# Performance work log

Hardware: AMD Instinct MI355X
Metric: run time of the kernel (lower is better)

Reference implementation:

```python
import jax, jax.numpy as jnp
import numpy as np

B, T, D, E, K, OUT = 512, 2048, 32, 64, 8, 1024  # batch, tokens, feat(=32 hardcoded), experts, top-k, expert out dim


def setup_inputs() -> dict:
    key = jax.random.key(0)
    k0, k1, k2, k3 = jax.random.split(key, 4)
    x = jax.random.normal(k0, (B, T, D), jnp.float32)
    gate_w = jax.random.normal(k1, (E, D), jnp.float32) / np.sqrt(D)
    gate_b = jnp.zeros((E,), jnp.float32)
    # stacked expert Linear(32*k -> OUT): weight [E, OUT, D*K], bias [E, OUT]
    expert_w = jax.random.normal(k2, (E, OUT, D * K), jnp.float32) / np.sqrt(D * K)
    expert_b = jnp.zeros((E, OUT), jnp.float32)
    # gumbel noise for multinomial-without-replacement sampling (Gumbel top-k trick)
    gumbel = jax.random.gumbel(k3, (B, E, T), jnp.float32)
    return {"x": x, "gate_w": gate_w, "gate_b": gate_b,
            "expert_w": expert_w, "expert_b": expert_b, "gumbel": gumbel}


def reference(x, gate_w, gate_b, expert_w, expert_b, gumbel):
    # gate logits [B,T,E]; softmax over TOKEN axis (dim=-2 in torch)
    logits = jnp.einsum('btd,ed->bte', x, gate_w) + gate_b
    logp = jax.nn.log_softmax(logits, axis=-2)          # [B,T,E]
    # g = probs transposed to [B,E,T]; multinomial(k, no replacement) == top-k of log p + Gumbel
    scores = jnp.transpose(logp, (0, 2, 1)) + gumbel    # [B,E,T]
    _, idx = jax.lax.top_k(scores, K)                   # [B,E,K] sampled token indices
    # gather k tokens per (batch, expert): [B,E,K,D]
    gathered = jnp.take_along_axis(x[:, None, :, :], idx[..., None], axis=2)
    inp = gathered.reshape(B, E, K * D)                 # token-major concat, matches torch reshape
    # grouped per-expert GEMM + bias -> [B,E,OUT]
    out = jnp.einsum('bef,eof->beo', inp, expert_w) + expert_b[None]
    return out
```

## Files before the change

### kernel.cpp

```cpp
#include <hip/hip_runtime.h>
#include <hip/hip_bf16.h>
#include <stdint.h>

#define Bb   512
#define Tt   2048
#define Dd   32
#define Ee   64
#define Kk   8
#define OUTn 1024

typedef __attribute__((ext_vector_type(4))) float f32x4;
typedef __attribute__((ext_vector_type(8))) short short8;
typedef __attribute__((ext_vector_type(4))) unsigned int uint4v;

static __device__ __forceinline__ uint32_t f2bf(float f) {
  uint32_t u = __float_as_uint(f);
  return (u + 0x7FFFu + ((u >> 16) & 1u)) >> 16;
}
static __device__ __forceinline__ uint32_t umax32(uint32_t a, uint32_t b){ return a > b ? a : b; }
static __device__ __forceinline__ uint32_t umin32(uint32_t a, uint32_t b){ return a < b ? a : b; }

__global__ __launch_bounds__(1024) void kA_select(
    const float* __restrict__ x,
    const float* __restrict__ gate_w,
    const float* __restrict__ gumbel,
    uint16_t* __restrict__ inp)
{
  const int b    = blockIdx.x;
  const int tid  = threadIdx.x;
  const int wave = tid >> 6;
  const int lane = tid & 63;
  const int l15  = lane & 15;
  const int l4   = lane >> 4;
  const int c    = wave & 3;
  const int q    = wave >> 2;

  __shared__ __attribute__((aligned(16))) float gbuf[16 * 1024];
  __shared__ uint32_t cand[Ee][32];

  short8 gfrag;
  {
    const float* gp = gate_w + (size_t)(c * 16 + l15) * Dd + l4 * 8;
    f32x4 g0 = *(const f32x4*)(gp);
    f32x4 g1 = *(const f32x4*)(gp + 4);
    gfrag[0] = (short)f2bf(g0[0]); gfrag[1] = (short)f2bf(g0[1]);
    gfrag[2] = (short)f2bf(g0[2]); gfrag[3] = (short)f2bf(g0[3]);
    gfrag[4] = (short)f2bf(g1[0]); gfrag[5] = (short)f2bf(g1[1]);
    gfrag[6] = (short)f2bf(g1[2]); gfrag[7] = (short)f2bf(g1[3]);
  }

  uint32_t s[4][8];
  #pragma unroll
  for (int r = 0; r < 4; ++r)
    #pragma unroll
    for (int j = 0; j < 8; ++j) s[r][j] = 0u;

  const float* gchunk = gumbel + ((size_t)b * Ee + c * 16) * Tt + q * 512;
  const int v0 = (lane >> 5) * Tt + (lane & 31);
  const int v1 = (lane >> 5) * Tt + ((lane & 31) ^ 16);
  const float* xq = x + ((size_t)b * Tt + q * 512 + l15) * Dd + l4 * 8;

  auto stage = [&](int st, int bf) {
    #pragma unroll
    for (int j = 0; j < 8; ++j) {
      const float* src = gchunk + j * 2 * Tt + st * 32 + (((j >> 1) & 1) ? v1 : v0);
      float* dst = &gbuf[wave * 1024 + bf * 512 + j * 64];
      __builtin_amdgcn_global_load_lds(
          (const __attribute__((address_space(1))) void*)src,
          (__attribute__((address_space(3))) void*)dst, 4, 0, 0);
    }
  };

  auto compute = [&](int st, int bf, f32x4 (&xv)[4]) {
    const int sbase = wave * 1024 + bf * 512;
    #pragma unroll
    for (int g = 0; g < 2; ++g) {
      f32x4 lo = xv[g * 2], hi = xv[g * 2 + 1];
      short8 bfr;
      bfr[0] = (short)f2bf(lo[0]); bfr[1] = (short)f2bf(lo[1]);
      bfr[2] = (short)f2bf(lo[2]); bfr[3] = (short)f2bf(lo[3]);
      bfr[4] = (short)f2bf(hi[0]); bfr[5] = (short)f2bf(hi[1]);
      bfr[6] = (short)f2bf(hi[2]); bfr[7] = (short)f2bf(hi[3]);
      f32x4 acc = {0.f, 0.f, 0.f, 0.f};
      acc = __builtin_amdgcn_mfma_f32_16x16x32_bf16(gfrag, bfr, acc, 0, 0, 0);
      const uint32_t tl = 2047u - (uint32_t)(q * 512 + st * 32 + g * 16 + l15);
      const int p = (g * 16 + l15) ^ ((l4 & 1) * 16);
      #pragma unroll
      for (int r = 0; r < 4; ++r) {
        float sc = acc[r] + gbuf[sbase + (l4 * 4 + r) * 32 + p];
        uint32_t u = __float_as_uint(sc);
        u = (u & 0x80000000u) ? ~u : (u | 0x80000000u);
        uint32_t key = (u & 0xFFFFF800u) | tl;
        uint32_t cc = umax32(s[r][7], key);
        uint32_t dd;
        dd = s[r][6]; s[r][7] = umin32(dd, cc); cc = umax32(dd, cc);
        dd = s[r][5]; s[r][6] = umin32(dd, cc); cc = umax32(dd, cc);
        dd = s[r][4]; s[r][5] = umin32(dd, cc); cc = umax32(dd, cc);
        dd = s[r][3]; s[r][4] = umin32(dd, cc); cc = umax32(dd, cc);
        dd = s[r][2]; s[r][3] = umin32(dd, cc); cc = umax32(dd, cc);
        dd = s[r][1]; s[r][2] = umin32(dd, cc); cc = umax32(dd, cc);
        dd = s[r][0]; s[r][1] = umin32(dd, cc); s[r][0] = umax32(dd, cc);
      }
    }
  };

  stage(0, 0);
  for (int i = 0; i < 16; ++i) {
    f32x4 xv[4];
    #pragma unroll
    for (int g = 0; g < 2; ++g)
      #pragma unroll
      for (int hv = 0; hv < 2; ++hv)
        xv[g * 2 + hv] = *(const f32x4*)(xq + (size_t)(i * 32 + g * 16) * Dd + hv * 4);
    if (i < 15) {
      stage(i + 1, (i + 1) & 1);
      asm volatile("s_waitcnt vmcnt(12)" ::: "memory");
    } else {
      asm volatile("s_waitcnt vmcnt(4)" ::: "memory");
    }
    __builtin_amdgcn_sched_barrier(0);
    compute(i, i & 1, xv);
  }

  #pragma unroll
  for (int r = 0; r < 4; ++r) {
    const int e_abs = c * 16 + l4 * 4 + r;
    #pragma unroll
    for (int rnd = 0; rnd < 8; ++rnd) {
      uint32_t cur = s[r][0];
      uint32_t mx = cur;
      mx = umax32(mx, (uint32_t)__shfl_xor((int)mx, 1));
      mx = umax32(mx, (uint32_t)__shfl_xor((int)mx, 2));
      mx = umax32(mx, (uint32_t)__shfl_xor((int)mx, 4));
      mx = umax32(mx, (uint32_t)__shfl_xor((int)mx, 8));
      if (l15 == rnd) cand[e_abs][q * 8 + rnd] = mx;
      const bool pop = (cur == mx);
      s[r][0] = pop ? s[r][1] : s[r][0];
      s[r][1] = pop ? s[r][2] : s[r][1];
      s[r][2] = pop ? s[r][3] : s[r][2];
      s[r][3] = pop ? s[r][4] : s[r][3];
      s[r][4] = pop ? s[r][5] : s[r][4];
      s[r][5] = pop ? s[r][6] : s[r][5];
      s[r][6] = pop ? s[r][7] : s[r][6];
      s[r][7] = pop ? 0u      : s[r][7];
    }
  }
  __syncthreads();

  #pragma unroll 1
  for (int el = 0; el < 4; ++el) {
    const int e = wave * 4 + el;
    const bool alive = lane < 32;
    uint32_t myT = 2047;
    double v = -1e300;
    if (alive) {
      uint32_t key = cand[e][lane];
      myT = 2047u - (key & 2047u);
      const float* xr = x + ((size_t)b * Tt + myT) * Dd;
      const float* gr = gate_w + (size_t)e * Dd;
      double a = 0.0;
      #pragma unroll
      for (int d = 0; d < Dd; ++d) a += (double)xr[d] * (double)gr[d];
      v = a + (double)gumbel[((size_t)b * Ee + e) * Tt + myT];
    }
    uint32_t ti = alive ? myT : 0xFFFFu;
    uint32_t ord[8];
    #pragma unroll
    for (int k = 0; k < 8; ++k) {
      double bv = v; uint32_t bt = ti;
      #pragma unroll
      for (int off = 1; off < 64; off <<= 1) {
        double   ov = __shfl_xor(bv, off);
        uint32_t ot = (uint32_t)__shfl_xor((int)bt, off);
        if (ov > bv || (ov == bv && ot < bt)) { bv = ov; bt = ot; }
      }
      ord[k] = bt;
      if (ti == bt) v = -1e300;
    }

    const int kk = lane >> 3, sub = lane & 7;
    uint32_t tk = ord[0];
    #pragma unroll
    for (int qq = 1; qq < 8; ++qq) tk = (kk == qq) ? ord[qq] : tk;
    const float* xs = x + ((size_t)b * Tt + tk) * Dd + sub * 4;
    f32x4 xv = *(const f32x4*)xs;
    uint32_t p0 = f2bf(xv[0]) | (f2bf(xv[1]) << 16);
    uint32_t p1 = f2bf(xv[2]) | (f2bf(xv[3]) << 16);
    uint32_t* dst = (uint32_t*)inp + ((((size_t)b * Ee + e) * 256) + kk * 32 + sub * 4) / 2;
    dst[0] = p0; dst[1] = p1;
  }
}

__global__ __launch_bounds__(256) void kB_gemm(
    const uint16_t* __restrict__ inp,
    const float* __restrict__ expert_w,
    const float* __restrict__ expert_b,
    float* __restrict__ out)
{
  const int bid = blockIdx.x;
  const int xcd = bid & 7;
  const int idx = bid >> 3;
  const int e   = xcd * 8 + (idx >> 5);
  const int rem = idx & 31;
  const int mb  = rem >> 3;
  const int nb  = rem & 7;
  const int b0 = mb * 128;
  const int o0 = nb * 128;
  const int tid  = threadIdx.x;
  const int wave = tid >> 6;
  const int lane = tid & 63;
  const int l15 = lane & 15, l4 = lane >> 4;
  const int wm = (wave & 1) * 64;
  const int wn = (wave >> 1) * 64;

  __shared__ __attribute__((aligned(16))) uint32_t Al[128 * 32];
  __shared__ __attribute__((aligned(16))) uint32_t Wl[128 * 32];

  f32x4 acc[4][4];
  #pragma unroll
  for (int i = 0; i < 4; ++i)
    #pragma unroll
    for (int j = 0; j < 4; ++j) acc[i][j] = (f32x4){0.f, 0.f, 0.f, 0.f};

  for (int ks = 0; ks < 4; ++ks) {
    #pragma unroll
    for (int i = 0; i < 4; ++i) {
      int gi = tid + i * 256;
      int m = gi >> 3, qq = gi & 7;
      const uint4v* src = (const uint4v*)(inp + ((size_t)(b0 + m) * Ee + e) * 256 + ks * 64 + qq * 8);
      *(uint4v*)&Al[m * 32 + ((qq ^ (m & 7)) * 4)] = *src;
    }
    #pragma unroll
    for (int i = 0; i < 4; ++i) {
      int gi = tid + i * 256;
      int o = gi >> 3, qq = gi & 7;
      const float* src = expert_w + ((size_t)e * OUTn + o0 + o) * 256 + ks * 64 + qq * 8;
      f32x4 w0 = *(const f32x4*)src;
      f32x4 w1 = *(const f32x4*)(src + 4);
      uint4v v;
      v[0] = f2bf(w0[0]) | (f2bf(w0[1]) << 16);
      v[1] = f2bf(w0[2]) | (f2bf(w0[3]) << 16);
      v[2] = f2bf(w1[0]) | (f2bf(w1[1]) << 16);
      v[3] = f2bf(w1[2]) | (f2bf(w1[3]) << 16);
      *(uint4v*)&Wl[o * 32 + ((qq ^ (o & 7)) * 4)] = v;
    }
    __syncthreads();

    short8 af[4][2], bf[4][2];
    #pragma unroll
    for (int mf = 0; mf < 4; ++mf)
      #pragma unroll
      for (int kb = 0; kb < 2; ++kb) {
        int row = wm + mf * 16 + l15;
        int g = kb * 4 + l4;
        af[mf][kb] = *(const short8*)&Al[row * 32 + ((g ^ (row & 7)) * 4)];
      }
    #pragma unroll
    for (int nf = 0; nf < 4; ++nf)
      #pragma unroll
      for (int kb = 0; kb < 2; ++kb) {
        int row = wn + nf * 16 + l15;
        int g = kb * 4 + l4;
        bf[nf][kb] = *(const short8*)&Wl[row * 32 + ((g ^ (row & 7)) * 4)];
      }
    #pragma unroll
    for (int mf = 0; mf < 4; ++mf)
      #pragma unroll
      for (int nf = 0; nf < 4; ++nf)
        #pragma unroll
        for (int kb = 0; kb < 2; ++kb)
          acc[mf][nf] = __builtin_amdgcn_mfma_f32_16x16x32_bf16(af[mf][kb], bf[nf][kb], acc[mf][nf], 0, 0, 0);
    __syncthreads();
  }

  #pragma unroll
  for (int nf = 0; nf < 4; ++nf) {
    const int ocol = o0 + wn + nf * 16 + l15;
    const float bias = expert_b[(size_t)e * OUTn + ocol];
    #pragma unroll
    for (int mf = 0; mf < 4; ++mf) {
      #pragma unroll
      for (int reg = 0; reg < 4; ++reg) {
        const int mrow = b0 + wm + mf * 16 + l4 * 4 + reg;
        out[((size_t)mrow * Ee + e) * OUTn + ocol] = acc[mf][nf][reg] + bias;
      }
    }
  }
}

extern "C" void kernel_launch(void* const* d_in, const int* in_sizes, int n_in,
                              void* d_out, int out_size, void* d_ws, size_t ws_size,
                              hipStream_t stream) {
  const float* x        = (const float*)d_in[0];
  const float* gate_w   = (const float*)d_in[1];
  const float* expert_w = (const float*)d_in[3];
  const float* expert_b = (const float*)d_in[4];
  const float* gumbel   = (const float*)d_in[5];

  uint16_t* inp = (uint16_t*)d_ws;

  kA_select<<<Bb, 1024, 0, stream>>>(x, gate_w, gumbel, inp);
  kB_gemm<<<2048, 256, 0, stream>>>(inp, expert_w, expert_b, (float*)d_out);
}
```

Before: 247.3 us.

## Halve select block size, stage x and gumbel via swizzled 16B LDS loads

The selection kernel now runs 512 threads per batch, with each wave covering 1024 tokens instead of 512. Both x and gumbel tiles are staged into XOR-swizzled LDS buffers using 16-byte global_load_lds, replacing 4-byte gumbel loads and direct x register loads. The per-lane sorted candidate list shrinks from 8 to 6 entries, so each lane sorts fewer values. The risk is in the smaller candidate list: if more than 6 of a lane's top tokens land in one expert, exact top-8 selection may miss them, though the candidates go through a later merge and exact rescoring.

```diff
diff --git a/kernel.cpp b/kernel.cpp
--- a/kernel.cpp
+++ b/kernel.cpp
@@ -20,7 +20,7 @@
 static __device__ __forceinline__ uint32_t umax32(uint32_t a, uint32_t b){ return a > b ? a : b; }
 static __device__ __forceinline__ uint32_t umin32(uint32_t a, uint32_t b){ return a < b ? a : b; }
 
-__global__ __launch_bounds__(1024) void kA_select(
+__global__ __launch_bounds__(512) void kA_select(
     const float* __restrict__ x,
     const float* __restrict__ gate_w,
     const float* __restrict__ gumbel,
@@ -33,10 +33,11 @@
   const int l15  = lane & 15;
   const int l4   = lane >> 4;
   const int c    = wave & 3;
-  const int q    = wave >> 2;
-
-  __shared__ __attribute__((aligned(16))) float gbuf[16 * 1024];
-  __shared__ uint32_t cand[Ee][32];
+  const int h    = wave >> 2;
+
+  __shared__ __attribute__((aligned(16))) float xbuf[8][2][1024];
+  __shared__ __attribute__((aligned(16))) float gbuf[8][2][512];
+  __shared__ uint32_t cand[Ee][16];
 
   short8 gfrag;
   {
@@ -49,52 +50,61 @@
     gfrag[6] = (short)f2bf(g1[2]); gfrag[7] = (short)f2bf(g1[3]);
   }
 
-  uint32_t s[4][8];
+  uint32_t s[4][6];
   #pragma unroll
   for (int r = 0; r < 4; ++r)
     #pragma unroll
-    for (int j = 0; j < 8; ++j) s[r][j] = 0u;
-
-  const float* gchunk = gumbel + ((size_t)b * Ee + c * 16) * Tt + q * 512;
-  const int v0 = (lane >> 5) * Tt + (lane & 31);
-  const int v1 = (lane >> 5) * Tt + ((lane & 31) ^ 16);
-  const float* xq = x + ((size_t)b * Tt + q * 512 + l15) * Dd + l4 * 8;
+    for (int j = 0; j < 6; ++j) s[r][j] = 0u;
+
+  const float* xbase  = x + ((size_t)b * Tt + h * 1024) * Dd;
+  const float* gchunk = gumbel + ((size_t)b * Ee + c * 16) * Tt + h * 1024;
+  const int    swz    = (lane & 7) ^ ((lane >> 3) & 7);
+  const int    lrow   = lane >> 3;
 
   auto stage = [&](int st, int bf) {
     #pragma unroll
-    for (int j = 0; j < 8; ++j) {
-      const float* src = gchunk + j * 2 * Tt + st * 32 + (((j >> 1) & 1) ? v1 : v0);
-      float* dst = &gbuf[wave * 1024 + bf * 512 + j * 64];
+    for (int j = 0; j < 4; ++j) {
+      const float* src = xbase + (size_t)(st * 32 + j * 8 + lrow) * Dd + swz * 4;
+      float* dst = &xbuf[wave][bf][j * 256];
       __builtin_amdgcn_global_load_lds(
           (const __attribute__((address_space(1))) void*)src,
-          (__attribute__((address_space(3))) void*)dst, 4, 0, 0);
+          (__attribute__((address_space(3))) void*)dst, 16, 0, 0);
+    }
+    #pragma unroll
+    for (int j = 0; j < 2; ++j) {
+      const float* src = gchunk + (size_t)(j * 8 + lrow) * Tt + st * 32 + swz * 4;
+      float* dst = &gbuf[wave][bf][j * 256];
+      __builtin_amdgcn_global_load_lds(
+          (const __attribute__((address_space(1))) void*)src,
+          (__attribute__((address_space(3))) void*)dst, 16, 0, 0);
     }
   };
 
-  auto compute = [&](int st, int bf, f32x4 (&xv)[4]) {
-    const int sbase = wave * 1024 + bf * 512;
+  auto compute = [&](int st, int bf) {
     #pragma unroll
     for (int g = 0; g < 2; ++g) {
-      f32x4 lo = xv[g * 2], hi = xv[g * 2 + 1];
+      const int t = g * 16 + l15;
+      const float* xr = &xbuf[wave][bf][t * 32];
+      f32x4 x0 = *(const f32x4*)(xr + (((l4 * 2 + 0) ^ (t & 7)) << 2));
+      f32x4 x1 = *(const f32x4*)(xr + (((l4 * 2 + 1) ^ (t & 7)) << 2));
       short8 bfr;
-      bfr[0] = (short)f2bf(lo[0]); bfr[1] = (short)f2bf(lo[1]);
-      bfr[2] = (short)f2bf(lo[2]); bfr[3] = (short)f2bf(lo[3]);
-      bfr[4] = (short)f2bf(hi[0]); bfr[5] = (short)f2bf(hi[1]);
-      bfr[6] = (short)f2bf(hi[2]); bfr[7] = (short)f2bf(hi[3]);
+      bfr[0] = (short)f2bf(x0[0]); bfr[1] = (short)f2bf(x0[1]);
+      bfr[2] = (short)f2bf(x0[2]); bfr[3] = (short)f2bf(x0[3]);
+      bfr[4] = (short)f2bf(x1[0]); bfr[5] = (short)f2bf(x1[1]);
+      bfr[6] = (short)f2bf(x1[2]); bfr[7] = (short)f2bf(x1[3]);
       f32x4 acc = {0.f, 0.f, 0.f, 0.f};
       acc = __builtin_amdgcn_mfma_f32_16x16x32_bf16(gfrag, bfr, acc, 0, 0, 0);
-      const uint32_t tl = 2047u - (uint32_t)(q * 512 + st * 32 + g * 16 + l15);
-      const int p = (g * 16 + l15) ^ ((l4 & 1) * 16);
+      const uint32_t tl = 2047u - (uint32_t)(h * 1024 + st * 32 + t);
       #pragma unroll
       for (int r = 0; r < 4; ++r) {
-        float sc = acc[r] + gbuf[sbase + (l4 * 4 + r) * 32 + p];
+        const int e7 = (l4 * 4 + r) & 7;
+        float gv = gbuf[wave][bf][(l4 * 4 + r) * 32 + (((t >> 2) ^ e7) << 2) + (t & 3)];
+        float sc = acc[r] + gv;
         uint32_t u = __float_as_uint(sc);
         u = (u & 0x80000000u) ? ~u : (u | 0x80000000u);
         uint32_t key = (u & 0xFFFFF800u) | tl;
-        uint32_t cc = umax32(s[r][7], key);
+        uint32_t cc = umax32(s[r][5], key);
         uint32_t dd;
-        dd = s[r][6]; s[r][7] = umin32(dd, cc); cc = umax32(dd, cc);
-        dd = s[r][5]; s[r][6] = umin32(dd, cc); cc = umax32(dd, cc);
         dd = s[r][4]; s[r][5] = umin32(dd, cc); cc = umax32(dd, cc);
         dd = s[r][3]; s[r][4] = umin32(dd, cc); cc = umax32(dd, cc);
         dd = s[r][2]; s[r][3] = umin32(dd, cc); cc = umax32(dd, cc);
@@ -105,21 +115,16 @@
   };
 
   stage(0, 0);
-  for (int i = 0; i < 16; ++i) {
-    f32x4 xv[4];
-    #pragma unroll
-    for (int g = 0; g < 2; ++g)
-      #pragma unroll
-      for (int hv = 0; hv < 2; ++hv)
-        xv[g * 2 + hv] = *(const f32x4*)(xq + (size_t)(i * 32 + g * 16) * Dd + hv * 4);
-    if (i < 15) {
+  #pragma unroll
+  for (int i = 0; i < 32; ++i) {
+    if (i < 31) {
       stage(i + 1, (i + 1) & 1);
-      asm volatile("s_waitcnt vmcnt(12)" ::: "memory");
+      asm volatile("s_waitcnt vmcnt(6)" ::: "memory");
     } else {
-      asm volatile("s_waitcnt vmcnt(4)" ::: "memory");
+      asm volatile("s_waitcnt vmcnt(0)" ::: "memory");
     }
     __builtin_amdgcn_sched_barrier(0);
-    compute(i, i & 1, xv);
+    compute(i, i & 1);
   }
 
   #pragma unroll
@@ -133,24 +138,22 @@
       mx = umax32(mx, (uint32_t)__shfl_xor((int)mx, 2));
       mx = umax32(mx, (uint32_t)__shfl_xor((int)mx, 4));
       mx = umax32(mx, (uint32_t)__shfl_xor((int)mx, 8));
-      if (l15 == rnd) cand[e_abs][q * 8 + rnd] = mx;
+      if (l15 == rnd) cand[e_abs][h * 8 + rnd] = mx;
       const bool pop = (cur == mx);
       s[r][0] = pop ? s[r][1] : s[r][0];
       s[r][1] = pop ? s[r][2] : s[r][1];
       s[r][2] = pop ? s[r][3] : s[r][2];
       s[r][3] = pop ? s[r][4] : s[r][3];
       s[r][4] = pop ? s[r][5] : s[r][4];
-      s[r][5] = pop ? s[r][6] : s[r][5];
-      s[r][6] = pop ? s[r][7] : s[r][6];
-      s[r][7] = pop ? 0u      : s[r][7];
+      s[r][5] = pop ? 0u      : s[r][5];
     }
   }
   __syncthreads();
 
   #pragma unroll 1
-  for (int el = 0; el < 4; ++el) {
-    const int e = wave * 4 + el;
-    const bool alive = lane < 32;
+  for (int el = 0; el < 8; ++el) {
+    const int e = wave * 8 + el;
+    const bool alive = lane < 16;
     uint32_t myT = 2047;
     double v = -1e300;
     if (alive) {
@@ -299,6 +302,6 @@
 
   uint16_t* inp = (uint16_t*)d_ws;
 
-  kA_select<<<Bb, 1024, 0, stream>>>(x, gate_w, gumbel, inp);
+  kA_select<<<Bb, 512, 0, stream>>>(x, gate_w, gumbel, inp);
   kB_gemm<<<2048, 256, 0, stream>>>(inp, expert_w, expert_b, (float*)d_out);
 }
```

New measurement: 397.7 us. +60.8%, slower.
